# Kernel optimization log

Measured on AMD Instinct MI355X. Metric: run time of the kernel, lower is better.

## Reference

```python
import jax, jax.numpy as jnp
import numpy as np

B, T, N, C = 16, 12, 2048, 64
WIN = 3                    # window_size
F = 3                      # len(filters) branches
NW = T - WIN + 1           # number of windows = 10


def setup_inputs() -> dict:
    key = jax.random.key(0)
    k0, k1, k2, k3, k4 = jax.random.split(key, 5)
    data = jax.random.normal(k0, (B, T, N, C), jnp.float32)
    # scale adj so aggregated features stay O(1)
    adj = jax.random.normal(k1, (WIN * N, WIN * N), jnp.float32) / np.float32(np.sqrt(WIN * N))
    temporal_emb = jax.random.normal(k2, (1, T, 1, C), jnp.float32) * 0.1
    spatial_emb = jax.random.normal(k3, (1, 1, N, C), jnp.float32) * 0.1
    # per-window, per-filter GLU linear: C -> 2C
    W = jax.random.normal(k4, (NW, F, C, 2 * C), jnp.float32) / np.float32(np.sqrt(C))
    b = jnp.zeros((NW, F, 2 * C), jnp.float32)
    return {"data": data, "adj": adj, "temporal_emb": temporal_emb,
            "spatial_emb": spatial_emb, "W": W, "b": b}


def reference(data, adj, temporal_emb, spatial_emb, W, b):
    # data: (B,T,N,C); adj: (3N,3N)
    x = data + temporal_emb + spatial_emb                     # (B,T,N,C)
    # sliding windows of 3 time steps, flattened to 3N nodes  # (B,NW,3N,C)
    wins = jnp.stack([x[:, i:i + WIN].reshape(B, WIN * N, C) for i in range(NW)], axis=1)
    # only the middle N rows of the bmm output survive the mid-step slice,
    # so aggregate with just those rows of adj (same math, less work)
    adj_mid = adj[(WIN - 1) // 2 * N:(WIN + 1) // 2 * N]      # (N, 3N)
    agg = jnp.einsum('mn,bwnc->bwmc', adj_mid, wins)          # (B,NW,N,C)
    # per-window per-filter linear C -> 2C, then GLU
    pre = jnp.einsum('bwnc,wfcd->bwfnd', agg, W) + b[None, :, :, None, :]  # (B,NW,F,N,2C)
    lhs, rhs = jnp.split(pre, 2, axis=-1)
    glu = lhs * jax.nn.sigmoid(rhs)                           # (B,NW,F,N,C)
    # max over filter branches -> (B, T-2, N, C)
    return jnp.max(glu, axis=2)
```

## Files before the change

kernel.cpp:

```cpp
#include <hip/hip_runtime.h>
#include <hip/hip_bf16.h>

#define B_ 16
#define T_ 12
#define N_ 2048
#define C_ 64
#define NW_ 10
#define K_ 6144

#define NT2_ 96
#define ABUF_E 16384
#define BBUF_E 20480
#define BUF2_E 36864

typedef __attribute__((ext_vector_type(8))) short bf16x8;
typedef __attribute__((ext_vector_type(4))) float f32x4;

__device__ __forceinline__ unsigned short f2bf(float f) {
  union { float f; unsigned int u; } v; v.f = f;
  unsigned int u = v.u;
  return (unsigned short)((u + 0x7FFFu + ((u >> 16) & 1u)) >> 16);
}

__device__ __forceinline__ void gload16(const void* g, void* l) {
  __builtin_amdgcn_global_load_lds(
      (const __attribute__((address_space(1))) unsigned int*)g,
      (__attribute__((address_space(3))) unsigned int*)l, 16, 0, 0);
}

template<int N>
__device__ __forceinline__ void vmw() {
  if constexpr (N == 10)     asm volatile("s_waitcnt vmcnt(10)" ::: "memory");
  else if constexpr (N == 8) asm volatile("s_waitcnt vmcnt(8)" ::: "memory");
  else if constexpr (N == 5) asm volatile("s_waitcnt vmcnt(5)" ::: "memory");
  else if constexpr (N == 4) asm volatile("s_waitcnt vmcnt(4)" ::: "memory");
  else                       asm volatile("s_waitcnt vmcnt(0)" ::: "memory");
}
__device__ __forceinline__ void lgkm0_fence() {
  asm volatile("s_waitcnt lgkmcnt(0)" ::: "memory");
  __builtin_amdgcn_sched_barrier(0);
}

__global__ __launch_bounds__(256) void prep_x2(const float* __restrict__ data,
                                               const float* __restrict__ temb,
                                               const float* __restrict__ semb,
                                               unsigned short* __restrict__ xbt2) {
  int idx = blockIdx.x * 256 + threadIdx.x;
  int q = idx & 511;
  int btnb = idx >> 9;
  int nb = btnb & 31;
  int bt = btnb >> 5;
  int t = bt % T_;
  int o = q >> 6, c = q & 63;
  int n0 = nb * 64 + o * 8;
  float te = temb[t * C_ + c];
  union { unsigned short s[8]; uint4 v; } pk;
#pragma unroll
  for (int e = 0; e < 8; ++e) {
    int n = n0 + e;
    float d = data[((size_t)bt * N_ + n) * C_ + c];
    float se = semb[(size_t)n * C_ + c];
    pk.s[e] = f2bf(d + te + se);
  }
  *(uint4*)(xbt2 + (size_t)idx * 8) = pk.v;
}

__global__ __launch_bounds__(256) void prep_adj2(const float* __restrict__ adj,
                                                 unsigned short* __restrict__ adjb2) {
  int idx = blockIdx.x * 256 + threadIdx.x;
  int s = idx & 2047;
  int bmt = idx >> 11;
  int t = bmt % NT2_;
  int bm = bmt / NT2_;
  int r = s & 15;
  int o = (s >> 4) & 7;
  int rg = s >> 7;
  int m = bm * 256 + rg * 16 + r;
  int k = t * 64 + o * 8;
  const float* src = adj + ((size_t)(N_ + m)) * K_ + k;
  float4 a = *(const float4*)src;
  float4 b4 = *(const float4*)(src + 4);
  union { unsigned short s8[8]; uint4 v; } pk;
  pk.s8[0] = f2bf(a.x);  pk.s8[1] = f2bf(a.y);  pk.s8[2] = f2bf(a.z);  pk.s8[3] = f2bf(a.w);
  pk.s8[4] = f2bf(b4.x); pk.s8[5] = f2bf(b4.y); pk.s8[6] = f2bf(b4.z); pk.s8[7] = f2bf(b4.w);
  *(uint4*)(adjb2 + (size_t)idx * 8) = pk.v;
}

__global__ __launch_bounds__(256) void prep_w(const float* __restrict__ W,
                                              unsigned short* __restrict__ wbt) {
  int idx = blockIdx.x * 256 + threadIdx.x;
  int c = idx & 63;
  int d = (idx >> 6) & 127;
  int wf = idx >> 13;
  float v = W[((size_t)wf * 64 + c) * 128 + d];
  wbt[idx] = f2bf(v);
}

struct SegCtx {
  const unsigned short* Abase;
  const unsigned short* Xroot;
  int lane, wid, wm, wn, l4, l15, fbase, bOffLane;
};

__device__ __forceinline__ void stage_group(const SegCtx& s, unsigned short* lds, int t, int kh) {
  unsigned short* buf = lds + (t & 1) * BUF2_E;
  int tp = t >> 5, nn = t & 31;
#pragma unroll
  for (int ci = 0; ci < 2; ++ci) {
    int rg = s.wid * 2 + ci;
    int off = (rg * 128 + kh * 64) * 8;
    gload16(s.Abase + (size_t)t * ABUF_E + off + s.lane * 8, buf + off);
  }
  unsigned short* Bb = buf + ABUF_E;
  const unsigned short* Xr = s.Xroot + ((size_t)tp * 32 + nn) * 4096;
  int c0 = (s.wid < 4) ? s.wid * 3 : 12 + (s.wid - 4) * 2;
  int nc = (s.wid < 4) ? 3 : 2;
  for (int ci = 0; ci < nc; ++ci) {
    int cg = c0 + ci;
    gload16(Xr + (size_t)(cg >> 2) * 131072 + kh * 2048 + (cg & 3) * 128 + s.bOffLane,
            Bb + cg * 1024 + kh * 512);
  }
}

__device__ __forceinline__ void frag_loads(const SegCtx& s, unsigned short* lds, int t, int kk,
                                           bf16x8 af[8], bf16x8 bfv[5]) {
  unsigned short* buf = lds + (t & 1) * BUF2_E;
  const unsigned short* Ab = buf;
  const unsigned short* Bb = buf + ABUF_E;
#pragma unroll
  for (int i = 0; i < 8; ++i)
    af[i] = *(const bf16x8*)(Ab + (s.wm * 8 + i) * 1024 + kk * 512 + s.fbase);
#pragma unroll
  for (int c = 0; c < 5; ++c)
    bfv[c] = *(const bf16x8*)(Bb + (s.wn * 5 + c) * 1024 + kk * 512 + s.fbase);
}

__device__ __forceinline__ void mfma_block(bf16x8 af[8], bf16x8 bfv[5], f32x4 acc[8][5]) {
  __builtin_amdgcn_s_setprio(1);
#pragma unroll
  for (int i = 0; i < 8; ++i)
#pragma unroll
    for (int c = 0; c < 5; ++c)
      acc[i][c] = __builtin_amdgcn_mfma_f32_16x16x32_bf16(af[i], bfv[c], acc[i][c], 0, 0, 0);
  __builtin_amdgcn_s_setprio(0);
}

__device__ __forceinline__ void vm_steady(const SegCtx& s) {
  if (s.wid < 4) vmw<10>(); else vmw<8>();
}

__global__ __launch_bounds__(512, 2) void gemm_agg(const unsigned short* __restrict__ adjb2,
                                                   const unsigned short* __restrict__ xbt2,
                                                   unsigned short* __restrict__ aggb) {
  __shared__ __align__(16) unsigned short lds[2 * BUF2_E];
  int bid = blockIdx.x;
  int bm = bid & 7;
  int rest = bid >> 3;
  int seg = rest & 1;
  int b = rest >> 1;
  int w0 = seg * 5;
  int tid = threadIdx.x;
  SegCtx s;
  s.lane = tid & 63; s.wid = tid >> 6;
  s.wm = s.wid >> 2; s.wn = s.wid & 3;
  s.l4 = s.lane >> 4; s.l15 = s.lane & 15;
  s.fbase = s.l4 * 128 + s.l15 * 8;
  s.bOffLane = s.l4 * 512 + s.l15 * 8;
  s.Abase = adjb2 + (size_t)bm * NT2_ * ABUF_E;
  s.Xroot = xbt2 + ((size_t)(b * T_ + w0)) * 32 * 4096;

  f32x4 acc[8][5];
#pragma unroll
  for (int i = 0; i < 8; ++i)
#pragma unroll
    for (int c = 0; c < 5; ++c) acc[i][c] = (f32x4)0.f;

  __builtin_amdgcn_sched_barrier(0);
  stage_group(s, lds, 0, 0);
  stage_group(s, lds, 0, 1);
  stage_group(s, lds, 1, 0);
  vm_steady(s);
  __builtin_amdgcn_s_barrier();
  __builtin_amdgcn_sched_barrier(0);

  for (int t = 0; t < NT2_; ++t) {
    bf16x8 af[8], bfv[5];
    frag_loads(s, lds, t, 0, af, bfv);
    if (t + 1 < NT2_) stage_group(s, lds, t + 1, 1);
    __builtin_amdgcn_s_barrier();
    lgkm0_fence();
    mfma_block(af, bfv, acc);
    if (t < NT2_ - 1) vm_steady(s); else vmw<0>();
    __builtin_amdgcn_s_barrier();
    __builtin_amdgcn_sched_barrier(0);
    frag_loads(s, lds, t, 1, af, bfv);
    if (t + 2 < NT2_) stage_group(s, lds, t + 2, 0);
    __builtin_amdgcn_s_barrier();
    lgkm0_fence();
    mfma_block(af, bfv, acc);
    if (t < NT2_ - 2) { vm_steady(s); }
    else if (t == NT2_ - 2) { if (s.wid < 4) vmw<5>(); else vmw<4>(); }
    if (t < NT2_ - 1) {
      __builtin_amdgcn_s_barrier();
      __builtin_amdgcn_sched_barrier(0);
    }
  }

  unsigned short* Ob0 = aggb + (size_t)(b * NW_ + w0) * N_ * C_;
#pragma unroll
  for (int c = 0; c < 5; ++c) {
    int col = s.wn * 80 + c * 16 + s.l15;
    int g = col >> 6, cc = col & 63;
    unsigned short* Ob = Ob0 + (size_t)g * N_ * C_ + cc;
#pragma unroll
    for (int i = 0; i < 8; ++i) {
      int n0 = bm * 256 + s.wm * 128 + i * 16 + s.l4 * 4;
#pragma unroll
      for (int q = 0; q < 4; ++q)
        Ob[(size_t)(n0 + q) * C_] = f2bf(acc[i][c][q]);
    }
  }
}

__global__ __launch_bounds__(256) void glu_out(const unsigned short* __restrict__ aggb,
                                               const unsigned short* __restrict__ wbt,
                                               const float* __restrict__ bias,
                                               float* __restrict__ out) {
  __shared__ __align__(16) unsigned short sW[3 * 128 * 64];
  int bn = blockIdx.x, bw = blockIdx.y;
  int w = bw % NW_;
  int tid = threadIdx.x, lane = tid & 63, wid = tid >> 6;
  int lrow8 = lane >> 3, jl = lane & 7;
  int l15 = lane & 15, l4 = lane >> 4;
  const unsigned short* Wsrc = wbt + (size_t)w * 3 * 128 * 64;
  for (int ci = 0; ci < 12; ++ci) {
    int chunk = wid * 12 + ci;
    int row = chunk * 8 + lrow8;
    int jg = jl ^ (row & 7);
    gload16(Wsrc + (size_t)row * 64 + jg * 8, &sW[chunk * 512]);
  }
  const unsigned short* Abase = aggb + ((size_t)bw * N_ + bn * 128 + wid * 32) * C_;
  bf16x8 af[2][2];
  for (int i = 0; i < 2; ++i)
    for (int kh = 0; kh < 2; ++kh)
      af[i][kh] = *(const bf16x8*)(Abase + (size_t)(i * 16 + l15) * C_ + kh * 32 + l4 * 8);
  __syncthreads();

  float omax[2][4][4];
  for (int i = 0; i < 2; ++i)
    for (int j = 0; j < 4; ++j)
      for (int r = 0; r < 4; ++r) omax[i][j][r] = -INFINITY;

  for (int f = 0; f < 3; ++f) {
    f32x4 acc[2][8];
    for (int i = 0; i < 2; ++i)
      for (int j = 0; j < 8; ++j) acc[i][j] = (f32x4)0.f;
    for (int kh = 0; kh < 2; ++kh) {
      int gchunk = kh * 4 + l4;
      for (int j = 0; j < 8; ++j) {
        int row = f * 128 + j * 16 + l15;
        int ch = gchunk ^ (row & 7);
        bf16x8 bfr = *(const bf16x8*)&sW[row * 64 + ch * 8];
        for (int i = 0; i < 2; ++i)
          acc[i][j] = __builtin_amdgcn_mfma_f32_16x16x32_bf16(af[i][kh], bfr, acc[i][j], 0, 0, 0);
      }
    }
    for (int j = 0; j < 4; ++j) {
      float bl = bias[(w * 3 + f) * 128 + j * 16 + l15];
      float br = bias[(w * 3 + f) * 128 + 64 + j * 16 + l15];
      for (int i = 0; i < 2; ++i)
        for (int r = 0; r < 4; ++r) {
          float lhs = acc[i][j][r] + bl;
          float rhs = acc[i][j + 4][r] + br;
          float g = lhs / (1.f + __expf(-rhs));
          omax[i][j][r] = fmaxf(omax[i][j][r], g);
        }
    }
  }
  float* Obase = out + ((size_t)bw * N_ + bn * 128 + wid * 32) * C_;
  for (int i = 0; i < 2; ++i)
    for (int j = 0; j < 4; ++j)
      for (int r = 0; r < 4; ++r)
        Obase[(size_t)(i * 16 + l4 * 4 + r) * C_ + j * 16 + l15] = omax[i][j][r];
}

extern "C" void kernel_launch(void* const* d_in, const int* in_sizes, int n_in,
                              void* d_out, int out_size, void* d_ws, size_t ws_size,
                              hipStream_t stream) {
  const float* data = (const float*)d_in[0];
  const float* adj  = (const float*)d_in[1];
  const float* temb = (const float*)d_in[2];
  const float* semb = (const float*)d_in[3];
  const float* W    = (const float*)d_in[4];
  const float* bias = (const float*)d_in[5];
  float* out = (float*)d_out;

  char* ws = (char*)d_ws;
  unsigned short* xbt2  = (unsigned short*)ws;
  unsigned short* adjb2 = (unsigned short*)(ws + 50331648);
  unsigned short* wbt   = (unsigned short*)(ws + 75497472);
  unsigned short* aggb  = (unsigned short*)(ws + 75988992);

  hipLaunchKernelGGL(prep_x2,   dim3(12288), dim3(256), 0, stream, data, temb, semb, xbt2);
  hipLaunchKernelGGL(prep_adj2, dim3(6144),  dim3(256), 0, stream, adj, adjb2);
  hipLaunchKernelGGL(prep_w,    dim3(960),   dim3(256), 0, stream, W, wbt);
  hipLaunchKernelGGL(gemm_agg,  dim3(256),   dim3(512), 0, stream, adjb2, xbt2, aggb);
  hipLaunchKernelGGL(glu_out,   dim3(16, 160), dim3(256), 0, stream, aggb, wbt, bias, out);
}
```

Before: 322.9 us.

## Software-pipeline A-fragment LDS reads and cut barriers per half-step in aggregation GEMM

Restructures the main GEMM loop so each half-K phase prefetches the low half of the next phase's A fragments into registers while the current MFMAs run, and drops the explicit lgkmcnt(0) fence plus one barrier per phase. Global-load waits are tightened to allow fewer outstanding stages before each barrier. The aim is to overlap LDS fragment reads with MFMA issue and reduce synchronization stalls, at the cost of extra live registers (four more bf16x8 vectors) and reliance on compiler-inserted LDS waits.

```diff
diff --git a/kernel.cpp b/kernel.cpp
--- a/kernel.cpp
+++ b/kernel.cpp
@@ -10,7 +10,6 @@
 
 #define NT2_ 96
 #define ABUF_E 16384
-#define BBUF_E 20480
 #define BUF2_E 36864
 
 typedef __attribute__((ext_vector_type(8))) short bf16x8;
@@ -30,15 +29,9 @@
 
 template<int N>
 __device__ __forceinline__ void vmw() {
-  if constexpr (N == 10)     asm volatile("s_waitcnt vmcnt(10)" ::: "memory");
-  else if constexpr (N == 8) asm volatile("s_waitcnt vmcnt(8)" ::: "memory");
-  else if constexpr (N == 5) asm volatile("s_waitcnt vmcnt(5)" ::: "memory");
+  if constexpr (N == 5)      asm volatile("s_waitcnt vmcnt(5)" ::: "memory");
   else if constexpr (N == 4) asm volatile("s_waitcnt vmcnt(4)" ::: "memory");
   else                       asm volatile("s_waitcnt vmcnt(0)" ::: "memory");
-}
-__device__ __forceinline__ void lgkm0_fence() {
-  asm volatile("s_waitcnt lgkmcnt(0)" ::: "memory");
-  __builtin_amdgcn_sched_barrier(0);
 }
 
 __global__ __launch_bounds__(256) void prep_x2(const float* __restrict__ data,
@@ -122,31 +115,54 @@
   }
 }
 
-__device__ __forceinline__ void frag_loads(const SegCtx& s, unsigned short* lds, int t, int kk,
-                                           bf16x8 af[8], bf16x8 bfv[5]) {
+__device__ __forceinline__ void vm_steady(const SegCtx& s) {
+  if (s.wid < 4) vmw<5>(); else vmw<4>();
+}
+
+template<int KK>
+__device__ __forceinline__ void phase_body(const SegCtx& s, unsigned short* lds, int t,
+                                           bf16x8 (&curLo)[4], bf16x8 (&nxtLo)[4],
+                                           f32x4 (&acc)[8][5]) {
+  if (t == NT2_ - 1) vmw<0>(); else vm_steady(s);
+  __builtin_amdgcn_s_barrier();
+  __builtin_amdgcn_sched_barrier(0);
+  if constexpr (KK == 0) { if (t + 1 < NT2_) stage_group(s, lds, t + 1, 1); }
+  else                   { if (t + 2 < NT2_) stage_group(s, lds, t + 2, 0); }
   unsigned short* buf = lds + (t & 1) * BUF2_E;
   const unsigned short* Ab = buf;
   const unsigned short* Bb = buf + ABUF_E;
-#pragma unroll
-  for (int i = 0; i < 8; ++i)
-    af[i] = *(const bf16x8*)(Ab + (s.wm * 8 + i) * 1024 + kk * 512 + s.fbase);
+  bf16x8 bfv[5], afhi[4];
 #pragma unroll
   for (int c = 0; c < 5; ++c)
-    bfv[c] = *(const bf16x8*)(Bb + (s.wn * 5 + c) * 1024 + kk * 512 + s.fbase);
-}
-
-__device__ __forceinline__ void mfma_block(bf16x8 af[8], bf16x8 bfv[5], f32x4 acc[8][5]) {
+    bfv[c] = *(const bf16x8*)(Bb + (s.wn * 5 + c) * 1024 + KK * 512 + s.fbase);
+#pragma unroll
+  for (int i = 0; i < 4; ++i)
+    afhi[i] = *(const bf16x8*)(Ab + (s.wm * 8 + 4 + i) * 1024 + KK * 512 + s.fbase);
+  if constexpr (KK == 0) {
+#pragma unroll
+    for (int i = 0; i < 4; ++i)
+      nxtLo[i] = *(const bf16x8*)(Ab + (s.wm * 8 + i) * 1024 + 512 + s.fbase);
+  } else {
+    if (t + 1 < NT2_) {
+      const unsigned short* nb = lds + ((t + 1) & 1) * BUF2_E;
+#pragma unroll
+      for (int i = 0; i < 4; ++i)
+        nxtLo[i] = *(const bf16x8*)(nb + (s.wm * 8 + i) * 1024 + s.fbase);
+    }
+  }
   __builtin_amdgcn_s_setprio(1);
 #pragma unroll
-  for (int i = 0; i < 8; ++i)
+  for (int i = 0; i < 4; ++i)
 #pragma unroll
     for (int c = 0; c < 5; ++c)
-      acc[i][c] = __builtin_amdgcn_mfma_f32_16x16x32_bf16(af[i], bfv[c], acc[i][c], 0, 0, 0);
+      acc[i][c] = __builtin_amdgcn_mfma_f32_16x16x32_bf16(curLo[i], bfv[c], acc[i][c], 0, 0, 0);
+#pragma unroll
+  for (int i = 0; i < 4; ++i)
+#pragma unroll
+    for (int c = 0; c < 5; ++c)
+      acc[4 + i][c] = __builtin_amdgcn_mfma_f32_16x16x32_bf16(afhi[i], bfv[c], acc[4 + i][c], 0, 0, 0);
   __builtin_amdgcn_s_setprio(0);
-}
-
-__device__ __forceinline__ void vm_steady(const SegCtx& s) {
-  if (s.wid < 4) vmw<10>(); else vmw<8>();
+  __builtin_amdgcn_sched_barrier(0);
 }
 
 __global__ __launch_bounds__(512, 2) void gemm_agg(const unsigned short* __restrict__ adjb2,
@@ -183,27 +199,14 @@
   __builtin_amdgcn_s_barrier();
   __builtin_amdgcn_sched_barrier(0);
 
+  bf16x8 P[4], Q[4];
+#pragma unroll
+  for (int i = 0; i < 4; ++i)
+    P[i] = *(const bf16x8*)(lds + (s.wm * 8 + i) * 1024 + s.fbase);
+
   for (int t = 0; t < NT2_; ++t) {
-    bf16x8 af[8], bfv[5];
-    frag_loads(s, lds, t, 0, af, bfv);
-    if (t + 1 < NT2_) stage_group(s, lds, t + 1, 1);
-    __builtin_amdgcn_s_barrier();
-    lgkm0_fence();
-    mfma_block(af, bfv, acc);
-    if (t < NT2_ - 1) vm_steady(s); else vmw<0>();
-    __builtin_amdgcn_s_barrier();
-    __builtin_amdgcn_sched_barrier(0);
-    frag_loads(s, lds, t, 1, af, bfv);
-    if (t + 2 < NT2_) stage_group(s, lds, t + 2, 0);
-    __builtin_amdgcn_s_barrier();
-    lgkm0_fence();
-    mfma_block(af, bfv, acc);
-    if (t < NT2_ - 2) { vm_steady(s); }
-    else if (t == NT2_ - 2) { if (s.wid < 4) vmw<5>(); else vmw<4>(); }
-    if (t < NT2_ - 1) {
-      __builtin_amdgcn_s_barrier();
-      __builtin_amdgcn_sched_barrier(0);
-    }
+    phase_body<0>(s, lds, t, P, Q, acc);
+    phase_body<1>(s, lds, t, Q, P, acc);
   }
 
   unsigned short* Ob0 = aggb + (size_t)(b * NW_ + w0) * N_ * C_;
```

Result: no change. 325.1 us (+0.7%).
